# Kernel tuning notes

Hardware: AMD Instinct MI355X
Metric: run time of the kernel (lower is better)

Reference implementation:

```python
import jax, jax.numpy as jnp
from jax import lax
import numpy as np

N_BLOCKS = 5; C = 256; K = 1024; NQ = 8; NRES = 4; B = 2; T = 65536


def conv1d(x, w, b, stride=1, padding=0, dilation=1):
    # x: [N,C,T], w: [O,I,k]
    y = lax.conv_general_dilated(x, w, (stride,), [(padding, padding)],
                                 rhs_dilation=(dilation,),
                                 dimension_numbers=('NCH', 'OIH', 'NCH'))
    return y + b[None, :, None]


def conv_transpose1d(x, w, b):
    # PyTorch ConvTranspose1d(k=4, s=2, p=1); w: [in, out, 4]
    wk = jnp.swapaxes(jnp.flip(w, -1), 0, 1)  # [out, in, 4]
    y = lax.conv_general_dilated(x, wk, (1,), [(2, 2)], lhs_dilation=(2,),
                                 dimension_numbers=('NCH', 'OIH', 'NCH'))
    return y + b[None, :, None]


def residual_model(x, w0, b0, w1, b1, dil):
    # ReLU -> dilated conv3 -> ReLU -> conv3
    h = conv1d(jax.nn.relu(x), w0, b0, padding=dil, dilation=dil)
    h = conv1d(jax.nn.relu(h), w1, b1, padding=1)
    return h


def encoder(x, d0w, d0b, dw, db, rw, rb):
    for i in range(N_BLOCKS):
        if i == 0:
            x = conv1d(x, d0w, d0b, stride=2, padding=1)
        else:
            x = conv1d(x, dw[i - 1], db[i - 1], stride=2, padding=1)
        for j in range(NRES):
            dil = 3 ** (j + 1)
            # ResidualBlock.forward: x + model(x)
            x = x + residual_model(x, rw[i, j, 0], rb[i, j, 0], rw[i, j, 1], rb[i, j, 1], dil)
    return x


def decoder(x, rw, rb, uw, ub, ulw, ulb):
    for i in range(N_BLOCKS):
        for j in range(NRES):
            dil = 3 ** (j + 1)
            # DecoderBlock: x = x + ResidualBlock(x) = x + (x + model(x))
            x = x + (x + residual_model(x, rw[i, j, 0], rb[i, j, 0], rw[i, j, 1], rb[i, j, 1], dil))
        if i == N_BLOCKS - 1:
            x = conv_transpose1d(x, ulw, ulb)
        else:
            x = conv_transpose1d(x, uw[i], ub[i])
    return x


def rvq(emb, rvq_sum, rvq_usage):
    # emb: [N, C]; eval-mode residual VQ (no EMA update)
    q = jnp.zeros_like(emb)
    commit = jnp.asarray(0.0, emb.dtype)
    codes = []
    for i in range(NQ):
        cb = rvq_sum[i] / jnp.clip(rvq_usage[i], 1e-5, None)[:, None]  # [K, C]
        res = emb - q
        # argmin of squared distance over codebook rows (||res||^2 constant per column)
        scores = jnp.sum(cb * cb, axis=1)[:, None] - 2.0 * (cb @ res.T)  # [K, N]
        c = jnp.argmin(scores, axis=0)
        eq = cb[c]  # [N, C]
        eq_st = res + lax.stop_gradient(eq - res)  # straight-through
        commit = commit + jnp.mean((lax.stop_gradient(eq_st) - res) ** 2)
        q = q + eq_st
        codes.append(c.astype(jnp.int32))
    return jnp.stack(codes, axis=1), q, commit


def setup_inputs() -> dict:
    key = jax.random.key(0)
    ks = iter(jax.random.split(key, 16))

    def W(shape, fan_in):
        return (jax.random.normal(next(ks), shape, jnp.float32) / np.float32(np.sqrt(fan_in)))

    return {
        'x': jax.random.normal(next(ks), (B, 1, T), jnp.float32),
        'enc_down0_w': W((C, 1, 4), 4),
        'enc_down0_b': jnp.zeros((C,), jnp.float32),
        'enc_down_w': W((N_BLOCKS - 1, C, C, 4), C * 4),
        'enc_down_b': jnp.zeros((N_BLOCKS - 1, C), jnp.float32),
        'enc_res_w': W((N_BLOCKS, NRES, 2, C, C, 3), C * 3),
        'enc_res_b': jnp.zeros((N_BLOCKS, NRES, 2, C), jnp.float32),
        'dec_res_w': W((N_BLOCKS, NRES, 2, C, C, 3), C * 3),
        'dec_res_b': jnp.zeros((N_BLOCKS, NRES, 2, C), jnp.float32),
        'dec_up_w': W((N_BLOCKS - 1, C, C, 4), C * 4),
        'dec_up_b': jnp.zeros((N_BLOCKS - 1, C), jnp.float32),
        'dec_up_last_w': W((C, 1, 4), C * 4),
        'dec_up_last_b': jnp.zeros((1,), jnp.float32),
        'rvq_sum': jax.random.normal(next(ks), (NQ, K, C), jnp.float32) * 0.1,
        'rvq_usage': jnp.ones((NQ, K), jnp.float32),
    }


def reference(x, enc_down0_w, enc_down0_b, enc_down_w, enc_down_b, enc_res_w, enc_res_b,
              dec_res_w, dec_res_b, dec_up_w, dec_up_b, dec_up_last_w, dec_up_last_b,
              rvq_sum, rvq_usage):
    z = encoder(x, enc_down0_w, enc_down0_b, enc_down_w, enc_down_b, enc_res_w, enc_res_b)
    Bz, Cz, Tz = z.shape
    emb = jnp.transpose(z, (0, 2, 1)).reshape(Bz * Tz, Cz)  # (b t) c
    codes, q, commit = rvq(emb, rvq_sum, rvq_usage)
    zq = jnp.transpose(q.reshape(Bz, Tz, Cz), (0, 2, 1))  # b c t
    recon = decoder(zq, dec_res_w, dec_res_b, dec_up_w, dec_up_b, dec_up_last_w, dec_up_last_b)
    return recon, codes, commit
```

## Files before the change

kernel.cpp:

```cpp
#include <hip/hip_runtime.h>
#include <cstdint>

#define DEVFN static __device__ __forceinline__
typedef unsigned short ushort_t;
typedef unsigned int uint_t;
typedef short short8 __attribute__((ext_vector_type(8)));
typedef float f32x4 __attribute__((ext_vector_type(4)));

DEVFN float bf2f(ushort_t h) { return __uint_as_float(((uint_t)h) << 16); }
DEVFN ushort_t bfhi(float f) {
    uint_t u = __float_as_uint(f);
    u += 0x7fffu + ((u >> 16) & 1u);
    return (ushort_t)(u >> 16);
}
DEVFN void fsplit(float f, ushort_t& h, ushort_t& l) {
    h = bfhi(f);
    l = bfhi(f - bf2f(h));
}
DEVFN void relu_pair(uint_t& h, uint_t& l) {
    float f0 = bf2f((ushort_t)(h & 0xffffu)) + bf2f((ushort_t)(l & 0xffffu));
    float f1 = bf2f((ushort_t)(h >> 16)) + bf2f((ushort_t)(l >> 16));
    if (f0 <= 0.f) { h &= 0xffff0000u; l &= 0xffff0000u; }
    if (f1 <= 0.f) { h &= 0x0000ffffu; l &= 0x0000ffffu; }
}
DEVFN int xcd_swz(int bx, int gx) {
    return ((gx & 7) == 0) ? ((bx & 7) * (gx >> 3) + (bx >> 3)) : bx;
}

__global__ __launch_bounds__(256)
void wprep3_k(const float* __restrict__ erw, const float* __restrict__ drw,
              ushort_t* __restrict__ wH, ushort_t* __restrict__ wL)
{
    const int gid = blockIdx.x * 256 + threadIdx.x;
    const int conv = gid >> 16;
    const int rem  = gid & 65535;
    const int co = rem >> 8, ci = rem & 255;
    const float* src = (conv < 40) ? (erw + (size_t)conv * 196608)
                                   : (drw + (size_t)(conv - 40) * 196608);
    const float* p = src + ((size_t)co * 256 + ci) * 3;
    ushort_t* oh = wH + (size_t)conv * 196608 + rem;
    ushort_t* ol = wL + (size_t)conv * 196608 + rem;
#pragma unroll
    for (int k = 0; k < 3; ++k) {
        ushort_t h, l; fsplit(p[k], h, l);
        oh[k * 65536] = h; ol[k * 65536] = l;
    }
}

__global__ __launch_bounds__(256)
void wprep4_k(const float* __restrict__ edw, const float* __restrict__ duw,
              ushort_t* __restrict__ wH, ushort_t* __restrict__ wL)
{
    const int gid = blockIdx.x * 256 + threadIdx.x;
    const int conv = gid >> 16;
    const int rem  = gid & 65535;
    const int co = rem >> 8, ci = rem & 255;
    ushort_t* oh = wH + (size_t)conv * 262144 + rem;
    ushort_t* ol = wL + (size_t)conv * 262144 + rem;
#pragma unroll
    for (int k = 0; k < 4; ++k) {
        float f;
        if (conv < 4)  f = edw[(size_t)conv * 262144 + ((size_t)co * 256 + ci) * 4 + k];
        else           f = duw[(size_t)(conv - 4) * 262144 + ((size_t)ci * 256 + co) * 4 + k];
        ushort_t h, l; fsplit(f, h, l);
        oh[k * 65536] = h; ol[k * 65536] = l;
    }
}

template<int TAPS, int STRIDE, bool RELU, int NT, int DMAX, bool DBUF>
__global__ __launch_bounds__(256, (NT >= 8) ? 2 : 3)
void convs_k(const ushort_t* __restrict__ inH, const ushort_t* __restrict__ inL,
             const ushort_t* __restrict__ wH, const ushort_t* __restrict__ wL,
             const float* __restrict__ bias,
             const ushort_t* __restrict__ srcH, const ushort_t* __restrict__ srcL,
             float alpha,
             ushort_t* __restrict__ outH, ushort_t* __restrict__ outL,
             int Lin, int Lout, int dil, int pad)
{
    constexpr int ROWS = NT * 16;
    constexpr int SMAX = STRIDE * (ROWS - 1) + (TAPS - 1) * DMAX + 1;
    constexpr int XSB  = SMAX * 80;
    constexpr int NEED = DBUF ? 4 * XSB : 2 * XSB;
    constexpr int ARENA = (NEED > 16640) ? NEED : 16640;
    static_assert(!DBUF || (4 * SMAX <= TAPS * 256), "prefetch item budget");
    __shared__ __align__(16) char sarena[ARENA];

    const int tid = threadIdx.x;
    const int b = blockIdx.z;
    const int t0 = xcd_swz(blockIdx.x, gridDim.x) * ROWS;
    const int wave = tid >> 6, lane = tid & 63;
    const int quad = lane >> 4, lr = lane & 15;
    const int cow = wave * 64;
    const size_t inbase = (size_t)b * Lin * 256;
    const int S = STRIDE * (ROWS - 1) + (TAPS - 1) * dil + 1;
    const int g0 = STRIDE * t0 - pad;

    f32x4 acc[4][NT];
#pragma unroll
    for (int m = 0; m < 4; ++m)
#pragma unroll
        for (int n = 0; n < NT; ++n) acc[m][n] = (f32x4)0.f;

    if constexpr (DBUF) {
        ushort_t (*xsH0)[40] = (ushort_t(*)[40])(sarena);
        ushort_t (*xsL0)[40] = (ushort_t(*)[40])(sarena + XSB);
        ushort_t (*xsH1)[40] = (ushort_t(*)[40])(sarena + 2 * XSB);
        ushort_t (*xsL1)[40] = (ushort_t(*)[40])(sarena + 3 * XSB);
        for (int idx = tid; idx < S * 4; idx += 256) {
            const int s = idx >> 2, p = idx & 3;
            const int t = g0 + s;
            uint4 hv = make_uint4(0, 0, 0, 0), lv = hv;
            if (t >= 0 && t < Lin) {
                const size_t g = inbase + (size_t)t * 256 + p * 8;
                hv = *(const uint4*)(inH + g);
                lv = *(const uint4*)(inL + g);
                if (RELU) {
                    relu_pair(hv.x, lv.x); relu_pair(hv.y, lv.y);
                    relu_pair(hv.z, lv.z); relu_pair(hv.w, lv.w);
                }
            }
            *(uint4*)&xsH0[s][p * 8] = hv;
            *(uint4*)&xsL0[s][p * 8] = lv;
        }
        __syncthreads();
        for (int chunk = 0; chunk < 8; ++chunk) {
            const int ci0 = chunk * 32;
            ushort_t (*xsH)[40] = (chunk & 1) ? xsH1 : xsH0;
            ushort_t (*xsL)[40] = (chunk & 1) ? xsL1 : xsL0;
            ushort_t (*xnH)[40] = (chunk & 1) ? xsH0 : xsH1;
            ushort_t (*xnL)[40] = (chunk & 1) ? xsL0 : xsL1;
            const bool pf = (chunk < 7);
#pragma unroll
            for (int tap = 0; tap < TAPS; ++tap) {
                const ushort_t* wHt = wH + (size_t)tap * 65536 + ci0 + quad * 8;
                const ushort_t* wLt = wL + (size_t)tap * 65536 + ci0 + quad * 8;
                short8 aH[4], aL[4];
#pragma unroll
                for (int m = 0; m < 4; ++m) {
                    const int co = cow + m * 16 + lr;
                    aH[m] = *(const short8*)(wHt + co * 256);
                    aL[m] = *(const short8*)(wLt + co * 256);
                }
                const int idx = tap * 256 + tid;
                const int s = idx >> 2, p = idx & 3;
                const int tr = g0 + s;
                const bool inr = (idx < S * 4);
                uint4 hv = make_uint4(0, 0, 0, 0), lv = hv;
                if (pf && inr && tr >= 0 && tr < Lin) {
                    const size_t g = inbase + (size_t)tr * 256 + (ci0 + 32) + p * 8;
                    hv = *(const uint4*)(inH + g);
                    lv = *(const uint4*)(inL + g);
                }
                const int rb = tap * dil;
#pragma unroll
                for (int n = 0; n < NT; ++n) {
                    const int srow = STRIDE * (n * 16 + lr) + rb;
                    const short8 bH = *(const short8*)&xsH[srow][quad * 8];
                    const short8 bL = *(const short8*)&xsL[srow][quad * 8];
#pragma unroll
                    for (int m = 0; m < 4; ++m)
                        acc[m][n] = __builtin_amdgcn_mfma_f32_16x16x32_bf16(aH[m], bH, acc[m][n], 0, 0, 0);
#pragma unroll
                    for (int m = 0; m < 4; ++m)
                        acc[m][n] = __builtin_amdgcn_mfma_f32_16x16x32_bf16(aH[m], bL, acc[m][n], 0, 0, 0);
#pragma unroll
                    for (int m = 0; m < 4; ++m)
                        acc[m][n] = __builtin_amdgcn_mfma_f32_16x16x32_bf16(aL[m], bH, acc[m][n], 0, 0, 0);
                }
                if (pf && inr) {
                    if (RELU) {
                        relu_pair(hv.x, lv.x); relu_pair(hv.y, lv.y);
                        relu_pair(hv.z, lv.z); relu_pair(hv.w, lv.w);
                    }
                    *(uint4*)&xnH[s][p * 8] = hv;
                    *(uint4*)&xnL[s][p * 8] = lv;
                }
            }
            __syncthreads();
        }
    } else {
        ushort_t (*xsH)[40] = (ushort_t(*)[40])(sarena);
        ushort_t (*xsL)[40] = (ushort_t(*)[40])(sarena + XSB);
        for (int chunk = 0; chunk < 8; ++chunk) {
            const int ci0 = chunk * 32;
            __syncthreads();
            for (int idx = tid; idx < S * 4; idx += 256) {
                const int s = idx >> 2, p = idx & 3;
                const int t = g0 + s;
                uint4 hv = make_uint4(0, 0, 0, 0), lv = hv;
                if (t >= 0 && t < Lin) {
                    const size_t g = inbase + (size_t)t * 256 + ci0 + p * 8;
                    hv = *(const uint4*)(inH + g);
                    lv = *(const uint4*)(inL + g);
                    if (RELU) {
                        relu_pair(hv.x, lv.x); relu_pair(hv.y, lv.y);
                        relu_pair(hv.z, lv.z); relu_pair(hv.w, lv.w);
                    }
                }
                *(uint4*)&xsH[s][p * 8] = hv;
                *(uint4*)&xsL[s][p * 8] = lv;
            }
            __syncthreads();
#pragma unroll
            for (int tap = 0; tap < TAPS; ++tap) {
                const ushort_t* wHt = wH + (size_t)tap * 65536 + ci0 + quad * 8;
                const ushort_t* wLt = wL + (size_t)tap * 65536 + ci0 + quad * 8;
                short8 aH[4], aL[4];
#pragma unroll
                for (int m = 0; m < 4; ++m) {
                    const int co = cow + m * 16 + lr;
                    aH[m] = *(const short8*)(wHt + co * 256);
                    aL[m] = *(const short8*)(wLt + co * 256);
                }
                const int rb = tap * dil;
#pragma unroll
                for (int n = 0; n < NT; ++n) {
                    const int srow = STRIDE * (n * 16 + lr) + rb;
                    const short8 bH = *(const short8*)&xsH[srow][quad * 8];
                    const short8 bL = *(const short8*)&xsL[srow][quad * 8];
#pragma unroll
                    for (int m = 0; m < 4; ++m)
                        acc[m][n] = __builtin_amdgcn_mfma_f32_16x16x32_bf16(aH[m], bH, acc[m][n], 0, 0, 0);
#pragma unroll
                    for (int m = 0; m < 4; ++m)
                        acc[m][n] = __builtin_amdgcn_mfma_f32_16x16x32_bf16(aH[m], bL, acc[m][n], 0, 0, 0);
#pragma unroll
                    for (int m = 0; m < 4; ++m)
                        acc[m][n] = __builtin_amdgcn_mfma_f32_16x16x32_bf16(aL[m], bH, acc[m][n], 0, 0, 0);
                }
            }
        }
    }
    float4 bvv[4];
#pragma unroll
    for (int m = 0; m < 4; ++m)
        bvv[m] = *(const float4*)&bias[cow + m * 16 + quad * 4];
    __syncthreads();
    float (*ebuf)[260] = (float(*)[260])sarena;
#pragma unroll
    for (int n = 0; n < NT; ++n) {
#pragma unroll
        for (int m = 0; m < 4; ++m) {
            float4 v;
            v.x = acc[m][n][0] + bvv[m].x;
            v.y = acc[m][n][1] + bvv[m].y;
            v.z = acc[m][n][2] + bvv[m].z;
            v.w = acc[m][n][3] + bvv[m].w;
            *(float4*)&ebuf[lr][cow + m * 16 + quad * 4] = v;
        }
        __syncthreads();
        {
            const int row = tid >> 4;
            const int c00 = (tid & 15) * 4;
            const int t = t0 + n * 16 + row;
            const size_t gr = ((size_t)b * Lout + t) * 256;
#pragma unroll
            for (int rep = 0; rep < 4; ++rep) {
                const int col = c00 + rep * 64;
                float4 v = *(const float4*)&ebuf[row][col];
                if (alpha != 0.f) {
                    const ushort4 sh = *(const ushort4*)(srcH + gr + col);
                    const ushort4 sl = *(const ushort4*)(srcL + gr + col);
                    v.x += alpha * (bf2f(sh.x) + bf2f(sl.x));
                    v.y += alpha * (bf2f(sh.y) + bf2f(sl.y));
                    v.z += alpha * (bf2f(sh.z) + bf2f(sl.z));
                    v.w += alpha * (bf2f(sh.w) + bf2f(sl.w));
                }
                ushort4 oh, ol;
                fsplit(v.x, oh.x, ol.x); fsplit(v.y, oh.y, ol.y);
                fsplit(v.z, oh.z, ol.z); fsplit(v.w, oh.w, ol.w);
                *(ushort4*)(outH + gr + col) = oh;
                *(ushort4*)(outL + gr + col) = ol;
            }
        }
        __syncthreads();
    }
}

template<int NTc>
__global__ __launch_bounds__(256, 2)
void convt_k(const ushort_t* __restrict__ inH, const ushort_t* __restrict__ inL,
             const ushort_t* __restrict__ wH, const ushort_t* __restrict__ wL,
             const float* __restrict__ bias,
             ushort_t* __restrict__ outH, ushort_t* __restrict__ outL, int Lin)
{
    constexpr int ROWS = NTc * 16;
    constexpr int S = ROWS + 2;
    constexpr int XSB = S * 40 * 2;
    constexpr int ARENA = (2 * XSB > 33280) ? 2 * XSB : 33280;
    __shared__ __align__(16) char sarena[ARENA];
    ushort_t (*xsH)[40] = (ushort_t(*)[40])(sarena);
    ushort_t (*xsL)[40] = (ushort_t(*)[40])(sarena + XSB);

    const int tid = threadIdx.x;
    const int b = blockIdx.z;
    const int m0 = xcd_swz(blockIdx.x, gridDim.x) * ROWS;
    const int Lout = Lin * 2;
    const int wave = tid >> 6, lane = tid & 63;
    const int quad = lane >> 4, lr = lane & 15;
    const int cow = wave * 64;
    const size_t inbase = (size_t)b * Lin * 256;

    f32x4 acc[4][NTc][2];
#pragma unroll
    for (int m = 0; m < 4; ++m)
#pragma unroll
        for (int n = 0; n < NTc; ++n) { acc[m][n][0] = (f32x4)0.f; acc[m][n][1] = (f32x4)0.f; }

    for (int chunk = 0; chunk < 8; ++chunk) {
        const int ci0 = chunk * 32;
        __syncthreads();
        for (int idx = tid; idx < S * 4; idx += 256) {
            const int s = idx >> 2, p = idx & 3;
            const int t = m0 - 1 + s;
            uint4 hv = make_uint4(0, 0, 0, 0), lv = hv;
            if (t >= 0 && t < Lin) {
                const size_t g = inbase + (size_t)t * 256 + ci0 + p * 8;
                hv = *(const uint4*)(inH + g);
                lv = *(const uint4*)(inL + g);
            }
            *(uint4*)&xsH[s][p * 8] = hv;
            *(uint4*)&xsL[s][p * 8] = lv;
        }
        __syncthreads();
#pragma unroll
        for (int tap = 0; tap < 4; ++tap) {
            const int ph = (tap == 0 || tap == 2) ? 1 : 0;
            const int sh = (tap == 0) ? 1 : ((tap == 3) ? -1 : 0);
            const ushort_t* wHt = wH + (size_t)tap * 65536 + ci0 + quad * 8;
            const ushort_t* wLt = wL + (size_t)tap * 65536 + ci0 + quad * 8;
            short8 aH[4], aL[4];
#pragma unroll
            for (int m = 0; m < 4; ++m) {
                const int co = cow + m * 16 + lr;
                aH[m] = *(const short8*)(wHt + co * 256);
                aL[m] = *(const short8*)(wLt + co * 256);
            }
#pragma unroll
            for (int n = 0; n < NTc; ++n) {
                const int srow = n * 16 + lr + sh + 1;
                const short8 bH = *(const short8*)&xsH[srow][quad * 8];
                const short8 bL = *(const short8*)&xsL[srow][quad * 8];
#pragma unroll
                for (int m = 0; m < 4; ++m)
                    acc[m][n][ph] = __builtin_amdgcn_mfma_f32_16x16x32_bf16(aH[m], bH, acc[m][n][ph], 0, 0, 0);
#pragma unroll
                for (int m = 0; m < 4; ++m)
                    acc[m][n][ph] = __builtin_amdgcn_mfma_f32_16x16x32_bf16(aH[m], bL, acc[m][n][ph], 0, 0, 0);
#pragma unroll
                for (int m = 0; m < 4; ++m)
                    acc[m][n][ph] = __builtin_amdgcn_mfma_f32_16x16x32_bf16(aL[m], bH, acc[m][n][ph], 0, 0, 0);
            }
        }
    }
    float4 bvv[4];
#pragma unroll
    for (int m = 0; m < 4; ++m)
        bvv[m] = *(const float4*)&bias[cow + m * 16 + quad * 4];
    __syncthreads();
    float (*ebuf)[260] = (float(*)[260])sarena;
#pragma unroll
    for (int n = 0; n < NTc; ++n) {
#pragma unroll
        for (int m = 0; m < 4; ++m) {
#pragma unroll
            for (int ph = 0; ph < 2; ++ph) {
                float4 v;
                v.x = acc[m][n][ph][0] + bvv[m].x;
                v.y = acc[m][n][ph][1] + bvv[m].y;
                v.z = acc[m][n][ph][2] + bvv[m].z;
                v.w = acc[m][n][ph][3] + bvv[m].w;
                *(float4*)&ebuf[2 * lr + ph][cow + m * 16 + quad * 4] = v;
            }
        }
        __syncthreads();
        {
            const int baset = 2 * (m0 + n * 16);
#pragma unroll
            for (int h = 0; h < 8; ++h) {
                const int row = (tid >> 4) + 16 * (h >> 2);
                const int col = (tid & 15) * 4 + (h & 3) * 64;
                const int t = baset + row;
                const size_t gr = ((size_t)b * Lout + t) * 256 + col;
                float4 v = *(const float4*)&ebuf[row][col];
                ushort4 oh, ol;
                fsplit(v.x, oh.x, ol.x); fsplit(v.y, oh.y, ol.y);
                fsplit(v.z, oh.z, ol.z); fsplit(v.w, oh.w, ol.w);
                *(ushort4*)(outH + gr) = oh;
                *(ushort4*)(outL + gr) = ol;
            }
        }
        __syncthreads();
    }
}

__global__ __launch_bounds__(256)
void down0_k2(const float* __restrict__ x, const float* __restrict__ w,
              const float* __restrict__ bias,
              ushort_t* __restrict__ outH, ushort_t* __restrict__ outL)
{
    const int t = blockIdx.x;
    const int b = blockIdx.y;
    const int co = threadIdx.x;
    const float* xb = x + (size_t)b * 65536;
    const float4 wv = *(const float4*)(w + co * 4);
    float s = bias[co];
    const int ti0 = 2 * t - 1;
    if (ti0 >= 0)      s = fmaf(xb[ti0], wv.x, s);
    s = fmaf(xb[ti0 + 1], wv.y, s);
    s = fmaf(xb[ti0 + 2], wv.z, s);
    if (ti0 + 3 < 65536) s = fmaf(xb[ti0 + 3], wv.w, s);
    ushort_t h, l; fsplit(s, h, l);
    const size_t g = ((size_t)b * 32768 + t) * 256 + co;
    outH[g] = h; outL[g] = l;
}

__global__ __launch_bounds__(256)
void uplast_k2(const ushort_t* __restrict__ inH, const ushort_t* __restrict__ inL,
               const float* __restrict__ w, const float* __restrict__ bias,
               float* __restrict__ out, int Lin)
{
    const int m = blockIdx.x * 256 + threadIdx.x;
    const int b = blockIdx.y;
    const float bv = bias[0];
    float aE = bv, aO = bv;
    const size_t base = (size_t)b * Lin * 256;
    const ushort_t* r0H = inH + base + (size_t)m * 256;
    const ushort_t* r0L = inL + base + (size_t)m * 256;
    const bool hasM = (m > 0), hasP = (m + 1 < Lin);
    for (int c0 = 0; c0 < 256; c0 += 8) {
        uint4 h0 = *(const uint4*)(r0H + c0);
        uint4 l0 = *(const uint4*)(r0L + c0);
        uint4 hm = make_uint4(0,0,0,0), lm = hm, hp = hm, lp = hm;
        if (hasM) { hm = *(const uint4*)(r0H - 256 + c0); lm = *(const uint4*)(r0L - 256 + c0); }
        if (hasP) { hp = *(const uint4*)(r0H + 256 + c0); lp = *(const uint4*)(r0L + 256 + c0); }
        const uint_t* h0p = (const uint_t*)&h0; const uint_t* l0p = (const uint_t*)&l0;
        const uint_t* hmp = (const uint_t*)&hm; const uint_t* lmp = (const uint_t*)&lm;
        const uint_t* hpp = (const uint_t*)&hp; const uint_t* lpp = (const uint_t*)&lp;
#pragma unroll
        for (int e = 0; e < 4; ++e) {
#pragma unroll
            for (int half = 0; half < 2; ++half) {
                const int sh = half * 16;
                const int ci = c0 + e * 2 + half;
                const float x0  = bf2f((ushort_t)(h0p[e] >> sh)) + bf2f((ushort_t)(l0p[e] >> sh));
                const float xm1 = bf2f((ushort_t)(hmp[e] >> sh)) + bf2f((ushort_t)(lmp[e] >> sh));
                const float xp1 = bf2f((ushort_t)(hpp[e] >> sh)) + bf2f((ushort_t)(lpp[e] >> sh));
                const float4 wv = *(const float4*)(w + ci * 4);
                aE = fmaf(x0, wv.y, fmaf(xm1, wv.w, aE));
                aO = fmaf(xp1, wv.x, fmaf(x0, wv.z, aO));
            }
        }
    }
    *(float2*)(out + (size_t)b * 2 * Lin + 2 * m) = make_float2(aE, aO);
}

__global__ void emb_k(const ushort_t* __restrict__ H, const ushort_t* __restrict__ L,
                      float* __restrict__ emb)
{
    const size_t g = (size_t)blockIdx.x * 256 + threadIdx.x;
    emb[g] = bf2f(H[g]) + bf2f(L[g]);
}
__global__ void qsplit_k(const float* __restrict__ q,
                         ushort_t* __restrict__ H, ushort_t* __restrict__ L)
{
    const size_t g = (size_t)blockIdx.x * 256 + threadIdx.x;
    ushort_t h, l; fsplit(q[g], h, l);
    H[g] = h; L[g] = l;
}

__global__ __launch_bounds__(256)
void rvq_cb_k(const float* __restrict__ sum, const float* __restrict__ usage,
              float* __restrict__ cb, float* __restrict__ cbT,
              float* __restrict__ cbn, int iq)
{
    const int k = blockIdx.x, c = threadIdx.x;
    const float den = fmaxf(usage[iq * 1024 + k], 1e-5f);
    const float v = sum[((size_t)iq * 1024 + k) * 256 + c] / den;
    cb[(size_t)k * 256 + c] = v;
    cbT[(size_t)c * 1024 + k] = v;
    float s = v * v;
    for (int off = 32; off; off >>= 1) s += __shfl_down(s, off, 64);
    __shared__ float ls[4];
    if ((c & 63) == 0) ls[c >> 6] = s;
    __syncthreads();
    if (c == 0) cbn[k] = ls[0] + ls[1] + ls[2] + ls[3];
}

DEVFN unsigned int ordbits(float f)
{
    unsigned u = __float_as_uint(f);
    return (u & 0x80000000u) ? ~u : (u | 0x80000000u);
}
DEVFN unsigned long long shfl_xor_u64(unsigned long long v, int mask)
{
    int lo = (int)(v & 0xffffffffull), hi = (int)(v >> 32);
    lo = __shfl_xor(lo, mask, 64);
    hi = __shfl_xor(hi, mask, 64);
    return ((unsigned long long)(unsigned)hi << 32) | (unsigned)lo;
}

__global__ __launch_bounds__(256)
void rvq_argmin_upd_k(const float* __restrict__ emb, float* __restrict__ q,
                      const float* __restrict__ cb, const float* __restrict__ cbT,
                      const float* __restrict__ cbn,
                      int* __restrict__ codes, float* __restrict__ codes_out,
                      float* __restrict__ commit, int iq)
{
    const int n0 = blockIdx.x * 16;
    const int tid = threadIdx.x;
    __shared__ float res[16][256];
    for (int idx = tid; idx < 16 * 256; idx += 256) {
        int nl = idx >> 8, c = idx & 255;
        size_t g = (size_t)(n0 + nl) * 256 + c;
        res[nl][c] = emb[g] - q[g];
    }
    __syncthreads();
    float dot[16][4];
#pragma unroll
    for (int nl = 0; nl < 16; ++nl)
#pragma unroll
        for (int j = 0; j < 4; ++j) dot[nl][j] = 0.f;

    const float* cbtp = cbT + tid * 4;
    for (int c = 0; c < 256; ++c) {
        const float4 cbv = *(const float4*)(cbtp + (size_t)c * 1024);
#pragma unroll
        for (int nl = 0; nl < 16; ++nl) {
            const float r = res[nl][c];
            dot[nl][0] = fmaf(cbv.x, r, dot[nl][0]);
            dot[nl][1] = fmaf(cbv.y, r, dot[nl][1]);
            dot[nl][2] = fmaf(cbv.z, r, dot[nl][2]);
            dot[nl][3] = fmaf(cbv.w, r, dot[nl][3]);
        }
    }
    const float4 nrm = *(const float4*)(cbn + tid * 4);
    __shared__ unsigned long long wred[4][16];
    __shared__ int scode[16];
    const int wave = tid >> 6, lane = tid & 63;
#pragma unroll
    for (int nl = 0; nl < 16; ++nl) {
        float s0 = nrm.x - 2.f * dot[nl][0];
        float s1 = nrm.y - 2.f * dot[nl][1];
        float s2 = nrm.z - 2.f * dot[nl][2];
        float s3 = nrm.w - 2.f * dot[nl][3];
        unsigned long long key =
            ((unsigned long long)ordbits(s0) << 32) | (unsigned)(tid * 4 + 0);
        unsigned long long k1 =
            ((unsigned long long)ordbits(s1) << 32) | (unsigned)(tid * 4 + 1);
        unsigned long long k2 =
            ((unsigned long long)ordbits(s2) << 32) | (unsigned)(tid * 4 + 2);
        unsigned long long k3 =
            ((unsigned long long)ordbits(s3) << 32) | (unsigned)(tid * 4 + 3);
        if (k1 < key) key = k1;
        if (k2 < key) key = k2;
        if (k3 < key) key = k3;
        for (int off = 32; off; off >>= 1) {
            unsigned long long o = shfl_xor_u64(key, off);
            if (o < key) key = o;
        }
        if (lane == 0) wred[wave][nl] = key;
    }
    __syncthreads();
    if (tid < 16) {
        unsigned long long bkey = wred[0][tid];
        if (wred[1][tid] < bkey) bkey = wred[1][tid];
        if (wred[2][tid] < bkey) bkey = wred[2][tid];
        if (wred[3][tid] < bkey) bkey = wred[3][tid];
        const int code = (int)(bkey & 0xffffffffull);
        scode[tid] = code;
        codes[(size_t)(n0 + tid) * 8 + iq] = code;
        codes_out[(size_t)(n0 + tid) * 8 + iq] = (float)code;
    }
    __syncthreads();
    float csum = 0.f;
#pragma unroll 4
    for (int nl = 0; nl < 16; ++nl) {
        const int code = scode[nl];
        const float cbv = cb[(size_t)code * 256 + tid];
        const float r = res[nl][tid];
        const size_t g = (size_t)(n0 + nl) * 256 + tid;
        q[g] = emb[g] - r + cbv;
        const float e = cbv - r;
        csum = fmaf(e, e, csum);
    }
    for (int off = 32; off; off >>= 1) csum += __shfl_down(csum, off, 64);
    __shared__ float ls2[4];
    if ((tid & 63) == 0) ls2[tid >> 6] = csum;
    __syncthreads();
    if (tid == 0) atomicAdd(commit, ls2[0] + ls2[1] + ls2[2] + ls2[3]);
}

__global__ void commit_write_k(const float* __restrict__ commit, float* __restrict__ out)
{
    out[0] = commit[0] * (1.f / (4096.f * 256.f));
}

extern "C" void kernel_launch(void* const* d_in, const int* in_sizes, int n_in,
                              void* d_out, int out_size, void* d_ws, size_t ws_size,
                              hipStream_t stream)
{
    const float* x    = (const float*)d_in[0];
    const float* ed0w = (const float*)d_in[1];
    const float* ed0b = (const float*)d_in[2];
    const float* edw  = (const float*)d_in[3];
    const float* edb  = (const float*)d_in[4];
    const float* erw  = (const float*)d_in[5];
    const float* erb  = (const float*)d_in[6];
    const float* drw  = (const float*)d_in[7];
    const float* drb  = (const float*)d_in[8];
    const float* duw  = (const float*)d_in[9];
    const float* dub  = (const float*)d_in[10];
    const float* dulw = (const float*)d_in[11];
    const float* dulb = (const float*)d_in[12];
    const float* rsum = (const float*)d_in[13];
    const float* rusg = (const float*)d_in[14];
    float* out = (float*)d_out;

    char* base = (char*)d_ws;
    size_t o = 0;
    ushort_t* wH3 = (ushort_t*)(base + o); o += 31457280;
    ushort_t* wL3 = (ushort_t*)(base + o); o += 31457280;
    ushort_t* w4H = (ushort_t*)(base + o); o += 4194304;
    ushort_t* w4L = (ushort_t*)(base + o); o += 4194304;
    ushort_t* AH  = (ushort_t*)(base + o); o += 33554432;
    ushort_t* AL  = (ushort_t*)(base + o); o += 33554432;
    ushort_t* BH  = (ushort_t*)(base + o); o += 33554432;
    ushort_t* BL  = (ushort_t*)(base + o); o += 33554432;
    float* emb    = (float*)(base + o);    o += 4194304;
    float* q      = (float*)(base + o);    o += 4194304;
    float* commit = (float*)(base + o);    o += 64;
    float* cb     = (float*)(base + o);    o += 1048576;
    float* cbT    = (float*)(base + o);    o += 1048576;
    float* cbn    = (float*)(base + o);    o += 4096;
    int*   codes  = (int*)(base + o);      o += 131072;

    static const int DIL[4] = {3, 9, 27, 81};

    hipMemsetAsync(q, 0, 4194304 + 64, stream);

    wprep3_k<<<20480, 256, 0, stream>>>(erw, drw, wH3, wL3);
    wprep4_k<<<2048, 256, 0, stream>>>(edw, duw, w4H, w4L);

    auto conv3 = [&](const ushort_t* iH, const ushort_t* iL,
                     const ushort_t* wh, const ushort_t* wl, const float* bb,
                     const ushort_t* sH, const ushort_t* sL, float alpha,
                     ushort_t* oH, ushort_t* oL, int L, int d) {
        const bool db = (d <= 27);
        if (L >= 16384) {
            if (db) convs_k<3, 1, true, 8, 27, true><<<dim3(L / 128, 1, 2), 256, 0, stream>>>(
                        iH, iL, wh, wl, bb, sH, sL, alpha, oH, oL, L, L, d, d);
            else    convs_k<3, 1, true, 8, 81, false><<<dim3(L / 128, 1, 2), 256, 0, stream>>>(
                        iH, iL, wh, wl, bb, sH, sL, alpha, oH, oL, L, L, d, d);
        } else if (L >= 8192) {
            if (db) convs_k<3, 1, true, 4, 27, true><<<dim3(L / 64, 1, 2), 256, 0, stream>>>(
                        iH, iL, wh, wl, bb, sH, sL, alpha, oH, oL, L, L, d, d);
            else    convs_k<3, 1, true, 4, 81, false><<<dim3(L / 64, 1, 2), 256, 0, stream>>>(
                        iH, iL, wh, wl, bb, sH, sL, alpha, oH, oL, L, L, d, d);
        } else if (L >= 4096) {
            if (db) convs_k<3, 1, true, 2, 27, true><<<dim3(L / 32, 1, 2), 256, 0, stream>>>(
                        iH, iL, wh, wl, bb, sH, sL, alpha, oH, oL, L, L, d, d);
            else    convs_k<3, 1, true, 2, 81, false><<<dim3(L / 32, 1, 2), 256, 0, stream>>>(
                        iH, iL, wh, wl, bb, sH, sL, alpha, oH, oL, L, L, d, d);
        } else {
            if (db) convs_k<3, 1, true, 1, 27, true><<<dim3(L / 16, 1, 2), 256, 0, stream>>>(
                        iH, iL, wh, wl, bb, sH, sL, alpha, oH, oL, L, L, d, d);
            else    convs_k<3, 1, true, 1, 81, false><<<dim3(L / 16, 1, 2), 256, 0, stream>>>(
                        iH, iL, wh, wl, bb, sH, sL, alpha, oH, oL, L, L, d, d);
        }
    };

    down0_k2<<<dim3(32768, 2), 256, 0, stream>>>(x, ed0w, ed0b, AH, AL);
    int L = 32768;
    for (int i = 0; i < 5; ++i) {
        if (i > 0) {
            const ushort_t* wh = w4H + (size_t)(i - 1) * 262144;
            const ushort_t* wl = w4L + (size_t)(i - 1) * 262144;
            const int Lout = L / 2;
            if (Lout >= 16384)
                convs_k<4, 2, false, 8, 1, false><<<dim3(Lout / 128, 1, 2), 256, 0, stream>>>(
                    AH, AL, wh, wl, edb + (i - 1) * 256, AH, AL, 0.f, BH, BL, L, Lout, 1, 1);
            else if (Lout >= 8192)
                convs_k<4, 2, false, 4, 1, false><<<dim3(Lout / 64, 1, 2), 256, 0, stream>>>(
                    AH, AL, wh, wl, edb + (i - 1) * 256, AH, AL, 0.f, BH, BL, L, Lout, 1, 1);
            else if (Lout >= 4096)
                convs_k<4, 2, false, 2, 1, false><<<dim3(Lout / 32, 1, 2), 256, 0, stream>>>(
                    AH, AL, wh, wl, edb + (i - 1) * 256, AH, AL, 0.f, BH, BL, L, Lout, 1, 1);
            else
                convs_k<4, 2, false, 1, 1, false><<<dim3(Lout / 16, 1, 2), 256, 0, stream>>>(
                    AH, AL, wh, wl, edb + (i - 1) * 256, AH, AL, 0.f, BH, BL, L, Lout, 1, 1);
            ushort_t* t;
            t = AH; AH = BH; BH = t;
            t = AL; AL = BL; BL = t;
            L = Lout;
        }
        for (int j = 0; j < 4; ++j) {
            const int d = DIL[j];
            const size_t u = (size_t)(i * 4 + j) * 2;
            conv3(AH, AL, wH3 + (u + 0) * 196608, wL3 + (u + 0) * 196608,
                  erb + (u + 0) * 256, AH, AL, 0.f, BH, BL, L, d);
            conv3(BH, BL, wH3 + (u + 1) * 196608, wL3 + (u + 1) * 196608,
                  erb + (u + 1) * 256, AH, AL, 1.f, AH, AL, L, 1);
        }
    }

    emb_k<<<4096, 256, 0, stream>>>(AH, AL, emb);
    for (int iq = 0; iq < 8; ++iq) {
        rvq_cb_k<<<1024, 256, 0, stream>>>(rsum, rusg, cb, cbT, cbn, iq);
        rvq_argmin_upd_k<<<256, 256, 0, stream>>>(emb, q, cb, cbT, cbn,
                                                  codes, out + 131072, commit, iq);
    }
    qsplit_k<<<4096, 256, 0, stream>>>(q, AH, AL);

    L = 2048;
    for (int i = 0; i < 5; ++i) {
        for (int j = 0; j < 4; ++j) {
            const int d = DIL[j];
            const size_t u = 40 + (size_t)(i * 4 + j) * 2;
            conv3(AH, AL, wH3 + (u + 0) * 196608, wL3 + (u + 0) * 196608,
                  drb + ((size_t)(i * 4 + j) * 2 + 0) * 256, AH, AL, 0.f, BH, BL, L, d);
            conv3(BH, BL, wH3 + (u + 1) * 196608, wL3 + (u + 1) * 196608,
                  drb + ((size_t)(i * 4 + j) * 2 + 1) * 256, AH, AL, 2.f, AH, AL, L, 1);
        }
        if (i < 4) {
            const ushort_t* wh = w4H + (size_t)(4 + i) * 262144;
            const ushort_t* wl = w4L + (size_t)(4 + i) * 262144;
            if (L >= 8192)
                convt_k<4><<<dim3(L / 64, 1, 2), 256, 0, stream>>>(
                    AH, AL, wh, wl, dub + i * 256, BH, BL, L);
            else if (L >= 4096)
                convt_k<2><<<dim3(L / 32, 1, 2), 256, 0, stream>>>(
                    AH, AL, wh, wl, dub + i * 256, BH, BL, L);
            else
                convt_k<1><<<dim3(L / 16, 1, 2), 256, 0, stream>>>(
                    AH, AL, wh, wl, dub + i * 256, BH, BL, L);
            ushort_t* t;
            t = AH; AH = BH; BH = t;
            t = AL; AL = BL; BL = t;
            L *= 2;
        } else {
            uplast_k2<<<dim3(L / 256, 2), 256, 0, stream>>>(AH, AL, dulw, dulb, out, L);
        }
    }

    commit_write_k<<<1, 1, 0, stream>>>(commit, out + 163840);
}
```

Before: 5.454 ms.

## Batch conv epilogue rows, raise MFMA priority, precompute all RVQ codebooks at once

After: 9.744 ms. 1.79x slower.

```diff
diff --git a/kernel.cpp b/kernel.cpp
--- a/kernel.cpp
+++ b/kernel.cpp
@@ -81,7 +81,8 @@
     constexpr int SMAX = STRIDE * (ROWS - 1) + (TAPS - 1) * DMAX + 1;
     constexpr int XSB  = SMAX * 80;
     constexpr int NEED = DBUF ? 4 * XSB : 2 * XSB;
-    constexpr int ARENA = (NEED > 16640) ? NEED : 16640;
+    constexpr int EMIN = (NT >= 2) ? 33280 : 16640;
+    constexpr int ARENA = (NEED > EMIN) ? NEED : EMIN;
     static_assert(!DBUF || (4 * SMAX <= TAPS * 256), "prefetch item budget");
     __shared__ __align__(16) char sarena[ARENA];
 
@@ -152,6 +153,7 @@
                     lv = *(const uint4*)(inL + g);
                 }
                 const int rb = tap * dil;
+                __builtin_amdgcn_s_setprio(1);
 #pragma unroll
                 for (int n = 0; n < NT; ++n) {
                     const int srow = STRIDE * (n * 16 + lr) + rb;
@@ -167,6 +169,7 @@
                     for (int m = 0; m < 4; ++m)
                         acc[m][n] = __builtin_amdgcn_mfma_f32_16x16x32_bf16(aL[m], bH, acc[m][n], 0, 0, 0);
                 }
+                __builtin_amdgcn_s_setprio(0);
                 if (pf && inr) {
                     if (RELU) {
                         relu_pair(hv.x, lv.x); relu_pair(hv.y, lv.y);
@@ -213,6 +216,7 @@
                     aL[m] = *(const short8*)(wLt + co * 256);
                 }
                 const int rb = tap * dil;
+                __builtin_amdgcn_s_setprio(1);
 #pragma unroll
                 for (int n = 0; n < NT; ++n) {
                     const int srow = STRIDE * (n * 16 + lr) + rb;
@@ -228,6 +232,7 @@
                     for (int m = 0; m < 4; ++m)
                         acc[m][n] = __builtin_amdgcn_mfma_f32_16x16x32_bf16(aL[m], bH, acc[m][n], 0, 0, 0);
                 }
+                __builtin_amdgcn_s_setprio(0);
             }
         }
     }
@@ -236,27 +241,29 @@
     for (int m = 0; m < 4; ++m)
         bvv[m] = *(const float4*)&bias[cow + m * 16 + quad * 4];
     __syncthreads();
-    float (*ebuf)[260] = (float(*)[260])sarena;
-#pragma unroll
-    for (int n = 0; n < NT; ++n) {
-#pragma unroll
-        for (int m = 0; m < 4; ++m) {
-            float4 v;
-            v.x = acc[m][n][0] + bvv[m].x;
-            v.y = acc[m][n][1] + bvv[m].y;
-            v.z = acc[m][n][2] + bvv[m].z;
-            v.w = acc[m][n][3] + bvv[m].w;
-            *(float4*)&ebuf[lr][cow + m * 16 + quad * 4] = v;
-        }
-        __syncthreads();
-        {
-            const int row = tid >> 4;
-            const int c00 = (tid & 15) * 4;
-            const int t = t0 + n * 16 + row;
-            const size_t gr = ((size_t)b * Lout + t) * 256;
-#pragma unroll
-            for (int rep = 0; rep < 4; ++rep) {
-                const int col = c00 + rep * 64;
+    if constexpr (NT >= 2) {
+        float (*ebuf)[260] = (float(*)[260])sarena;
+        for (int n2 = 0; n2 < NT; n2 += 2) {
+#pragma unroll
+            for (int half = 0; half < 2; ++half) {
+                const int n = n2 + half;
+#pragma unroll
+                for (int m = 0; m < 4; ++m) {
+                    float4 v;
+                    v.x = acc[m][n][0] + bvv[m].x;
+                    v.y = acc[m][n][1] + bvv[m].y;
+                    v.z = acc[m][n][2] + bvv[m].z;
+                    v.w = acc[m][n][3] + bvv[m].w;
+                    *(float4*)&ebuf[16 * half + lr][cow + m * 16 + quad * 4] = v;
+                }
+            }
+            __syncthreads();
+#pragma unroll
+            for (int h = 0; h < 8; ++h) {
+                const int row = (tid >> 4) + 16 * (h >> 2);
+                const int col = (tid & 15) * 4 + (h & 3) * 64;
+                const int t = t0 + n2 * 16 + row;
+                const size_t gr = ((size_t)b * Lout + t) * 256;
                 float4 v = *(const float4*)&ebuf[row][col];
                 if (alpha != 0.f) {
                     const ushort4 sh = *(const ushort4*)(srcH + gr + col);
@@ -272,8 +279,48 @@
                 *(ushort4*)(outH + gr + col) = oh;
                 *(ushort4*)(outL + gr + col) = ol;
             }
-        }
-        __syncthreads();
+            __syncthreads();
+        }
+    } else {
+        float (*ebuf)[260] = (float(*)[260])sarena;
+#pragma unroll
+        for (int n = 0; n < NT; ++n) {
+#pragma unroll
+            for (int m = 0; m < 4; ++m) {
+                float4 v;
+                v.x = acc[m][n][0] + bvv[m].x;
+                v.y = acc[m][n][1] + bvv[m].y;
+                v.z = acc[m][n][2] + bvv[m].z;
+                v.w = acc[m][n][3] + bvv[m].w;
+                *(float4*)&ebuf[lr][cow + m * 16 + quad * 4] = v;
+            }
+            __syncthreads();
+            {
+                const int row = tid >> 4;
+                const int c00 = (tid & 15) * 4;
+                const int t = t0 + n * 16 + row;
+                const size_t gr = ((size_t)b * Lout + t) * 256;
+#pragma unroll
+                for (int rep = 0; rep < 4; ++rep) {
+                    const int col = c00 + rep * 64;
+                    float4 v = *(const float4*)&ebuf[row][col];
+                    if (alpha != 0.f) {
+                        const ushort4 sh = *(const ushort4*)(srcH + gr + col);
+                        const ushort4 sl = *(const ushort4*)(srcL + gr + col);
+                        v.x += alpha * (bf2f(sh.x) + bf2f(sl.x));
+                        v.y += alpha * (bf2f(sh.y) + bf2f(sl.y));
+                        v.z += alpha * (bf2f(sh.z) + bf2f(sl.z));
+                        v.w += alpha * (bf2f(sh.w) + bf2f(sl.w));
+                    }
+                    ushort4 oh, ol;
+                    fsplit(v.x, oh.x, ol.x); fsplit(v.y, oh.y, ol.y);
+                    fsplit(v.z, oh.z, ol.z); fsplit(v.w, oh.w, ol.w);
+                    *(ushort4*)(outH + gr + col) = oh;
+                    *(ushort4*)(outL + gr + col) = ol;
+                }
+            }
+            __syncthreads();
+        }
     }
 }
 
@@ -336,6 +383,7 @@
                 aH[m] = *(const short8*)(wHt + co * 256);
                 aL[m] = *(const short8*)(wLt + co * 256);
             }
+            __builtin_amdgcn_s_setprio(1);
 #pragma unroll
             for (int n = 0; n < NTc; ++n) {
                 const int srow = n * 16 + lr + sh + 1;
@@ -351,6 +399,7 @@
                 for (int m = 0; m < 4; ++m)
                     acc[m][n][ph] = __builtin_amdgcn_mfma_f32_16x16x32_bf16(aL[m], bH, acc[m][n][ph], 0, 0, 0);
             }
+            __builtin_amdgcn_s_setprio(0);
         }
     }
     float4 bvv[4];
@@ -470,21 +519,21 @@
 }
 
 __global__ __launch_bounds__(256)
-void rvq_cb_k(const float* __restrict__ sum, const float* __restrict__ usage,
-              float* __restrict__ cb, float* __restrict__ cbT,
-              float* __restrict__ cbn, int iq)
-{
-    const int k = blockIdx.x, c = threadIdx.x;
+void rvq_cb_all_k(const float* __restrict__ sum, const float* __restrict__ usage,
+                  float* __restrict__ cb, float* __restrict__ cbT,
+                  float* __restrict__ cbn)
+{
+    const int k = blockIdx.x, iq = blockIdx.y, c = threadIdx.x;
     const float den = fmaxf(usage[iq * 1024 + k], 1e-5f);
     const float v = sum[((size_t)iq * 1024 + k) * 256 + c] / den;
-    cb[(size_t)k * 256 + c] = v;
-    cbT[(size_t)c * 1024 + k] = v;
+    cb[(size_t)iq * 262144 + (size_t)k * 256 + c] = v;
+    cbT[(size_t)iq * 262144 + (size_t)c * 1024 + k] = v;
     float s = v * v;
     for (int off = 32; off; off >>= 1) s += __shfl_down(s, off, 64);
     __shared__ float ls[4];
     if ((c & 63) == 0) ls[c >> 6] = s;
     __syncthreads();
-    if (c == 0) cbn[k] = ls[0] + ls[1] + ls[2] + ls[3];
+    if (c == 0) cbn[iq * 1024 + k] = ls[0] + ls[1] + ls[2] + ls[3];
 }
 
 DEVFN unsigned int ordbits(float f)
@@ -507,6 +556,9 @@
                       int* __restrict__ codes, float* __restrict__ codes_out,
                       float* __restrict__ commit, int iq)
 {
+    cb  += (size_t)iq * 262144;
+    cbT += (size_t)iq * 262144;
+    cbn += (size_t)iq * 1024;
     const int n0 = blockIdx.x * 16;
     const int tid = threadIdx.x;
     __shared__ float res[16][256];
@@ -630,9 +682,9 @@
     float* emb    = (float*)(base + o);    o += 4194304;
     float* q      = (float*)(base + o);    o += 4194304;
     float* commit = (float*)(base + o);    o += 64;
-    float* cb     = (float*)(base + o);    o += 1048576;
-    float* cbT    = (float*)(base + o);    o += 1048576;
-    float* cbn    = (float*)(base + o);    o += 4096;
+    float* cb     = (float*)(base + o);    o += 8388608;
+    float* cbT    = (float*)(base + o);    o += 8388608;
+    float* cbn    = (float*)(base + o);    o += 32768;
     int*   codes  = (int*)(base + o);      o += 131072;
 
     static const int DIL[4] = {3, 9, 27, 81};
@@ -705,8 +757,8 @@
     }
 
     emb_k<<<4096, 256, 0, stream>>>(AH, AL, emb);
+    rvq_cb_all_k<<<dim3(1024, 8), 256, 0, stream>>>(rsum, rusg, cb, cbT, cbn);
     for (int iq = 0; iq < 8; ++iq) {
-        rvq_cb_k<<<1024, 256, 0, stream>>>(rsum, rusg, cb, cbT, cbn, iq);
         rvq_argmin_upd_k<<<256, 256, 0, stream>>>(emb, q, cb, cbT, cbn,
                                                   codes, out + 131072, commit, iq);
     }
```
